# Kernel tuning notes

Measured on AMD Instinct MI355X. Metric: run time of the kernel, lower is better.

Reference implementation:

```python
import jax, jax.numpy as jnp
import numpy as np

B, S, D = 4, 2048, 512
H, DK, DV = 8, 64, 64
ALPHA = 0.6
MAX_ITERS = 3
EPS = 1e-9


def setup_inputs() -> dict:
    key = jax.random.key(0)
    ks = jax.random.split(key, 9)
    scale = 1.0 / np.sqrt(D)
    return {
        "x": jax.random.normal(ks[0], (B, S, D), dtype=jnp.float32),
        "Wq": jax.random.normal(ks[1], (D, H * DK), dtype=jnp.float32) * scale,
        "bq": jnp.zeros((H * DK,), dtype=jnp.float32),
        "Wk": jax.random.normal(ks[2], (D, H * DK), dtype=jnp.float32) * scale,
        "bk": jnp.zeros((H * DK,), dtype=jnp.float32),
        "Wv": jax.random.normal(ks[3], (D, H * DV), dtype=jnp.float32) * scale,
        "bv": jnp.zeros((H * DV,), dtype=jnp.float32),
        "Wo": jax.random.normal(ks[4], (H * DV, D), dtype=jnp.float32) * scale,
        "bo": jnp.zeros((D,), dtype=jnp.float32),
    }


def reference(x, Wq, bq, Wk, bk, Wv, bv, Wo, bo):
    # QKV projections -> [B, H, S, dk]
    q = (x @ Wq + bq).reshape(B, S, H, DK).transpose(0, 2, 1, 3)
    k = (x @ Wk + bk).reshape(B, S, H, DK).transpose(0, 2, 1, 3)
    v = (x @ Wv + bv).reshape(B, S, H, DV).transpose(0, 2, 1, 3)

    # scaled dot-product scores: [B, H, S, S]
    scores = jnp.einsum("bhqd,bhkd->bhqk", q, k) / jnp.sqrt(jnp.float32(DK))
    w = jax.nn.softmax(scores, axis=-1)

    # iterative sparsification: threshold_t = 1 / (alpha^t * N), then renormalize
    n = jnp.float32(S)
    for t in range(MAX_ITERS):
        thr = 1.0 / ((ALPHA ** t) * n)
        w = jnp.where(w >= thr, w, 0.0)
        w = w / (jnp.sum(w, axis=-1, keepdims=True) + EPS)

    # attend and project out
    out = jnp.einsum("bhqk,bhkd->bhqd", w, v)          # [B, H, S, dv]
    out = out.transpose(0, 2, 1, 3).reshape(B, S, H * DV)
    return out @ Wo + bo
```

## Files before the change

### kernel.cpp

```cpp
#include <hip/hip_runtime.h>
#include <hip/hip_bf16.h>
#include <math.h>

#define NB 4
#define NS 2048
#define ND 512
#define NH 8
#define NDK 64
#define NDV 64

typedef __attribute__((ext_vector_type(8))) short short8;
typedef __attribute__((ext_vector_type(4))) float f32x4;
typedef __attribute__((ext_vector_type(4))) unsigned int u32x4;

__device__ __forceinline__ unsigned short f2bfu(float f) {
  unsigned int u = __builtin_bit_cast(unsigned int, f);
  unsigned int rounding = 0x7fffu + ((u >> 16) & 1u);
  return (unsigned short)((u + rounding) >> 16);
}
__device__ __forceinline__ float bfu2f(unsigned short u) {
  return __builtin_bit_cast(float, (unsigned int)u << 16);
}


__global__ void k_make_xcat(const float* __restrict__ in, unsigned short* __restrict__ out,
                            int n4) {
  int i = blockIdx.x * 256 + threadIdx.x;
  if (i >= n4) return;
  int row = i >> 7, col = (i & 127) * 4;
  float4 f = reinterpret_cast<const float4*>(in)[i];
  ushort4 h, l;
  h.x = f2bfu(f.x); h.y = f2bfu(f.y); h.z = f2bfu(f.z); h.w = f2bfu(f.w);
  l.x = f2bfu(f.x - bfu2f(h.x)); l.y = f2bfu(f.y - bfu2f(h.y));
  l.z = f2bfu(f.z - bfu2f(h.z)); l.w = f2bfu(f.w - bfu2f(h.w));
  ushort4* o = reinterpret_cast<ushort4*>(out + (size_t)row * 1536);
  o[col / 4] = h;
  o[(col + 512) / 4] = h;
  o[(col + 1024) / 4] = l;
}

__global__ void k_transpose_split(const float* __restrict__ src, unsigned short* __restrict__ dst,
                                  int R, int C) {
  __shared__ float t[32][33];
  int bx = blockIdx.x * 32, by = blockIdx.y * 32;
  int tx = threadIdx.x, ty = threadIdx.y;
  for (int i = 0; i < 32; i += 8)
    t[ty + i][tx] = src[(size_t)(by + ty + i) * C + bx + tx];
  __syncthreads();
  for (int i = 0; i < 32; i += 8) {
    float f = t[tx][ty + i];
    unsigned short h = f2bfu(f);
    unsigned short l = f2bfu(f - bfu2f(h));
    size_t base = (size_t)(bx + ty + i) * (3 * R) + by + tx;
    dst[base] = h;
    dst[base + R] = l;
    dst[base + 2 * R] = h;
  }
}

template <int MODE>
__global__ __launch_bounds__(256) void k_gemm_nt(
    const unsigned short* __restrict__ A, const unsigned short* __restrict__ Bt,
    const float* __restrict__ bias, void* __restrict__ outp, unsigned short* __restrict__ outlo,
    int M, int N, int K) {
  __shared__ __align__(16) unsigned short As[64][88];
  __shared__ __align__(16) unsigned short Bs[64][88];
  const int tid = threadIdx.x;
  const int m0 = blockIdx.y * 64;
  const int n0 = blockIdx.x * 64;
  const int wave = tid >> 6, lane = tid & 63;
  const int lm = lane & 15, lg = lane >> 4;

  f32x4 acc[4];
  for (int n = 0; n < 4; n++) acc[n] = (f32x4){0.f, 0.f, 0.f, 0.f};

  for (int k0 = 0; k0 < K; k0 += 64) {
    for (int it = 0; it < 2; it++) {
      int c = tid + it * 256;
      int row = c >> 3, col = (c & 7) * 8;
      *reinterpret_cast<short8*>(&As[row][col]) =
          *reinterpret_cast<const short8*>(A + (size_t)(m0 + row) * K + k0 + col);
      *reinterpret_cast<short8*>(&Bs[row][col]) =
          *reinterpret_cast<const short8*>(Bt + (size_t)(n0 + row) * K + k0 + col);
    }
    __syncthreads();
#pragma unroll
    for (int ks = 0; ks < 2; ks++) {
      short8 a = *reinterpret_cast<const short8*>(&As[wave * 16 + lm][ks * 32 + lg * 8]);
#pragma unroll
      for (int n = 0; n < 4; n++) {
        short8 b = *reinterpret_cast<const short8*>(&Bs[n * 16 + lm][ks * 32 + lg * 8]);
        acc[n] = __builtin_amdgcn_mfma_f32_16x16x32_bf16(a, b, acc[n], 0, 0, 0);
      }
    }
    __syncthreads();
  }

#pragma unroll
  for (int n = 0; n < 4; n++) {
    int gn = n0 + n * 16 + lm;
    float bv = bias[gn];
#pragma unroll
    for (int r = 0; r < 4; r++) {
      int gm = m0 + wave * 16 + lg * 4 + r;
      float v = acc[n][r] + bv;
      if (MODE == 3) {
        reinterpret_cast<float*>(outp)[(size_t)gm * ND + gn] = v;
      } else {
        int b = gm >> 11, s = gm & (NS - 1);
        int h = gn >> 6, d = gn & 63;
        unsigned short hb = f2bfu(v);
        unsigned short lb = f2bfu(v - bfu2f(hb));
        size_t idx;
        if (MODE == 0)
          idx = (((size_t)b * NH + h) * NS + s) * NDK + d;
        else
          idx = (((size_t)b * NH + h) * NDV + d) * NS + s;
        reinterpret_cast<unsigned short*>(outp)[idx] = hb;
        outlo[idx] = lb;
      }
    }
  }
}

__global__ __launch_bounds__(512, 4) void k_sparse_attn(
    const unsigned short* __restrict__ Qh, const unsigned short* __restrict__ Ql,
    const unsigned short* __restrict__ Kh, const unsigned short* __restrict__ Kl,
    const unsigned short* __restrict__ Vth, const unsigned short* __restrict__ Vtl,
    unsigned short* __restrict__ attn) {
  __shared__ float part[5][8][16];
  __shared__ __align__(16) float red[8][16][68];

  const int tid = threadIdx.x;
  const int wave = tid >> 6, lane = tid & 63;
  const int lm = lane & 15, lg = lane >> 4;

  const int orig = blockIdx.x;
  const int blk = (orig & 7) * 512 + (orig >> 3);
  const int qt = blk & (NS / 16 - 1);
  const int bh = blk >> 7;
  const int q0 = qt * 16;

  const size_t qoff = ((size_t)bh * NS + q0) * NDK;
  const unsigned short* Kph = Kh + (size_t)bh * NS * NDK;
  const unsigned short* Kpl = Kl + (size_t)bh * NS * NDK;
  const unsigned short* Vph = Vth + (size_t)bh * NDV * NS;
  const unsigned short* Vpl = Vtl + (size_t)bh * NDV * NS;
  const int kvbase = wave * 256;

  f32x4 st[16];
  {
    short8 qh0 = *reinterpret_cast<const short8*>(Qh + qoff + lm * NDK + lg * 8);
    short8 qh1 = *reinterpret_cast<const short8*>(Qh + qoff + lm * NDK + 32 + lg * 8);
    short8 ql0 = *reinterpret_cast<const short8*>(Ql + qoff + lm * NDK + lg * 8);
    short8 ql1 = *reinterpret_cast<const short8*>(Ql + qoff + lm * NDK + 32 + lg * 8);
#pragma unroll
    for (int kt = 0; kt < 16; kt++) {
      size_t ko = (size_t)(kvbase + kt * 16) * NDK;
      const unsigned short* kh = Kph + ko + lm * NDK + lg * 8;
      const unsigned short* kl = Kpl + ko + lm * NDK + lg * 8;
      short8 ah0 = *reinterpret_cast<const short8*>(kh);
      short8 ah1 = *reinterpret_cast<const short8*>(kh + 32);
      short8 al0 = *reinterpret_cast<const short8*>(kl);
      short8 al1 = *reinterpret_cast<const short8*>(kl + 32);
      f32x4 a0 = (f32x4){0.f, 0.f, 0.f, 0.f};
      f32x4 a1 = (f32x4){0.f, 0.f, 0.f, 0.f};
      a0 = __builtin_amdgcn_mfma_f32_16x16x32_bf16(ah0, qh0, a0, 0, 0, 0);
      a1 = __builtin_amdgcn_mfma_f32_16x16x32_bf16(ah1, qh1, a1, 0, 0, 0);
      a0 = __builtin_amdgcn_mfma_f32_16x16x32_bf16(al0, qh0, a0, 0, 0, 0);
      a1 = __builtin_amdgcn_mfma_f32_16x16x32_bf16(al1, qh1, a1, 0, 0, 0);
      a0 = __builtin_amdgcn_mfma_f32_16x16x32_bf16(ah0, ql0, a0, 0, 0, 0);
      a1 = __builtin_amdgcn_mfma_f32_16x16x32_bf16(ah1, ql1, a1, 0, 0, 0);
      st[kt] = (a0 + a1) * 0.125f;
    }
  }

  float cut, inv;
  {
    float m = -1e30f;
#pragma unroll
    for (int kt = 0; kt < 16; kt++)
      m = fmaxf(m, fmaxf(fmaxf(st[kt][0], st[kt][1]), fmaxf(st[kt][2], st[kt][3])));
    m = fmaxf(m, __shfl_xor(m, 16));
    m = fmaxf(m, __shfl_xor(m, 32));
    if (lg == 0) part[0][wave][lm] = m;
    __syncthreads();
    float gm = -1e30f;
#pragma unroll
    for (int w = 0; w < 8; w++) gm = fmaxf(gm, part[0][w][lm]);

    float E = 0.f;
#pragma unroll
    for (int kt = 0; kt < 16; kt++) {
#pragma unroll
      for (int j = 0; j < 4; j++) {
        float e = __expf(st[kt][j] - gm);
        st[kt][j] = e;
        E += e;
      }
    }
    E += __shfl_xor(E, 16);
    E += __shfl_xor(E, 32);
    if (lg == 0) part[1][wave][lm] = E;
    __syncthreads();
    float gE = 0.f;
#pragma unroll
    for (int w = 0; w < 8; w++) gE += part[1][w][lm];

    const float thr[3] = {1.0f / 2048.0f, 1.0f / (0.6f * 2048.0f), 1.0f / (0.36f * 2048.0f)};
    float Dd = 1.0f;
    cut = 0.f;
#pragma unroll
    for (int t = 0; t < 3; t++) {
      cut = fmaxf(cut, thr[t] * Dd * gE);
      float S = 0.f;
#pragma unroll
      for (int kt = 0; kt < 16; kt++) {
#pragma unroll
        for (int j = 0; j < 4; j++) S += (st[kt][j] >= cut) ? st[kt][j] : 0.f;
      }
      S += __shfl_xor(S, 16);
      S += __shfl_xor(S, 32);
      if (lg == 0) part[2 + t][wave][lm] = S;
      __syncthreads();
      float gS = 0.f;
#pragma unroll
      for (int w = 0; w < 8; w++) gS += part[2 + t][w][lm];
      Dd = gS / gE + 1e-9f * Dd;
    }
    inv = 1.0f / (gE * Dd);
  }

  unsigned int Hp[16][2], Lp[16][2];
#pragma unroll
  for (int kt = 0; kt < 16; kt++) {
#pragma unroll
    for (int rp = 0; rp < 2; rp++) {
      float w0 = st[kt][2 * rp], w1 = st[kt][2 * rp + 1];
      w0 = (w0 >= cut) ? w0 * inv : 0.f;
      w1 = (w1 >= cut) ? w1 * inv : 0.f;
      unsigned int h0 = f2bfu(w0), h1 = f2bfu(w1);
      Hp[kt][rp] = h0 | (h1 << 16);
      unsigned int l0 = f2bfu(w0 - bfu2f((unsigned short)h0));
      unsigned int l1 = f2bfu(w1 - bfu2f((unsigned short)h1));
      Lp[kt][rp] = l0 | (l1 << 16);
    }
  }

  {
    const int e_lane = lm + 32 * (lg & 1);
    const int o_lane = e_lane + 16;
    const bool selB = (lane & 32) != 0;
    f32x4 acc[4];
#pragma unroll
    for (int dt = 0; dt < 4; dt++) acc[dt] = (f32x4){0.f, 0.f, 0.f, 0.f};
#pragma unroll
    for (int wi = 0; wi < 8; wi++) {
      unsigned int a0 = (unsigned)__shfl((int)Hp[2 * wi][0], e_lane);
      unsigned int a1 = (unsigned)__shfl((int)Hp[2 * wi][1], e_lane);
      unsigned int a2 = (unsigned)__shfl((int)Hp[2 * wi][0], o_lane);
      unsigned int a3 = (unsigned)__shfl((int)Hp[2 * wi][1], o_lane);
      unsigned int b0 = (unsigned)__shfl((int)Hp[2 * wi + 1][0], e_lane);
      unsigned int b1 = (unsigned)__shfl((int)Hp[2 * wi + 1][1], e_lane);
      unsigned int b2 = (unsigned)__shfl((int)Hp[2 * wi + 1][0], o_lane);
      unsigned int b3 = (unsigned)__shfl((int)Hp[2 * wi + 1][1], o_lane);
      u32x4 hw = (u32x4){selB ? b0 : a0, selB ? b1 : a1, selB ? b2 : a2, selB ? b3 : a3};
      a0 = (unsigned)__shfl((int)Lp[2 * wi][0], e_lane);
      a1 = (unsigned)__shfl((int)Lp[2 * wi][1], e_lane);
      a2 = (unsigned)__shfl((int)Lp[2 * wi][0], o_lane);
      a3 = (unsigned)__shfl((int)Lp[2 * wi][1], o_lane);
      b0 = (unsigned)__shfl((int)Lp[2 * wi + 1][0], e_lane);
      b1 = (unsigned)__shfl((int)Lp[2 * wi + 1][1], e_lane);
      b2 = (unsigned)__shfl((int)Lp[2 * wi + 1][0], o_lane);
      b3 = (unsigned)__shfl((int)Lp[2 * wi + 1][1], o_lane);
      u32x4 lw = (u32x4){selB ? b0 : a0, selB ? b1 : a1, selB ? b2 : a2, selB ? b3 : a3};
      short8 Ah = __builtin_bit_cast(short8, hw);
      short8 Al = __builtin_bit_cast(short8, lw);
      const int co = kvbase + wi * 32 + lg * 8;
#pragma unroll
      for (int dt = 0; dt < 4; dt++) {
        short8 V0 = *reinterpret_cast<const short8*>(Vph + (size_t)(dt * 16 + lm) * NS + co);
        short8 V1 = *reinterpret_cast<const short8*>(Vpl + (size_t)(dt * 16 + lm) * NS + co);
        acc[dt] = __builtin_amdgcn_mfma_f32_16x16x32_bf16(Ah, V0, acc[dt], 0, 0, 0);
        acc[dt] = __builtin_amdgcn_mfma_f32_16x16x32_bf16(Ah, V1, acc[dt], 0, 0, 0);
        acc[dt] = __builtin_amdgcn_mfma_f32_16x16x32_bf16(Al, V0, acc[dt], 0, 0, 0);
      }
    }
#pragma unroll
    for (int dt = 0; dt < 4; dt++)
#pragma unroll
      for (int rr = 0; rr < 4; rr++) red[wave][lg * 4 + rr][dt * 16 + lm] = acc[dt][rr];
  }
  __syncthreads();

  {
    const int q = tid >> 5;
    const int dv0 = (tid & 31) * 2;
    const int b = bh >> 3, h = bh & 7;
    const int s = q0 + q;
    size_t base = ((size_t)b * NS + s) * 1536;
#pragma unroll
    for (int k2 = 0; k2 < 2; k2++) {
      int dv = dv0 + k2;
      float v = 0.f;
#pragma unroll
      for (int w = 0; w < 8; w++) v += red[w][q][dv];
      int c = h * 64 + dv;
      unsigned short hb = f2bfu(v);
      unsigned short lb = f2bfu(v - bfu2f(hb));
      attn[base + c] = hb;
      attn[base + c + 512] = hb;
      attn[base + c + 1024] = lb;
    }
  }
}


extern "C" void kernel_launch(void* const* d_in, const int* in_sizes, int n_in,
                              void* d_out, int out_size, void* d_ws, size_t ws_size,
                              hipStream_t stream) {
  const float* x  = (const float*)d_in[0];
  const float* Wq = (const float*)d_in[1];
  const float* bq = (const float*)d_in[2];
  const float* Wk = (const float*)d_in[3];
  const float* bk = (const float*)d_in[4];
  const float* Wv = (const float*)d_in[5];
  const float* bv = (const float*)d_in[6];
  const float* Wo = (const float*)d_in[7];
  const float* bo = (const float*)d_in[8];

  char* ws = (char*)d_ws;
  size_t off = 0;
  auto alloc = [&](size_t bytes) {
    char* p = ws + off;
    off += (bytes + 255) & ~(size_t)255;
    return p;
  };
  const int M = NB * NS;
  unsigned short* xcat = (unsigned short*)alloc((size_t)M * 1536 * 2);
  unsigned short* wqC  = (unsigned short*)alloc((size_t)512 * 1536 * 2);
  unsigned short* wkC  = (unsigned short*)alloc((size_t)512 * 1536 * 2);
  unsigned short* wvC  = (unsigned short*)alloc((size_t)512 * 1536 * 2);
  unsigned short* woC  = (unsigned short*)alloc((size_t)512 * 1536 * 2);
  unsigned short* Qhi  = (unsigned short*)alloc((size_t)M * 512 * 2);
  unsigned short* Qlo  = (unsigned short*)alloc((size_t)M * 512 * 2);
  unsigned short* Khi  = (unsigned short*)alloc((size_t)M * 512 * 2);
  unsigned short* Klo  = (unsigned short*)alloc((size_t)M * 512 * 2);
  unsigned short* Vthi = (unsigned short*)alloc((size_t)M * 512 * 2);
  unsigned short* Vtlo = (unsigned short*)alloc((size_t)M * 512 * 2);
  unsigned short* attn = xcat;

  k_make_xcat<<<(M * 512 / 4 + 255) / 256, 256, 0, stream>>>(x, xcat, M * 512 / 4);

  dim3 tg(16, 16), tb(32, 8);
  k_transpose_split<<<tg, tb, 0, stream>>>(Wq, wqC, ND, NH * NDK);
  k_transpose_split<<<tg, tb, 0, stream>>>(Wk, wkC, ND, NH * NDK);
  k_transpose_split<<<tg, tb, 0, stream>>>(Wv, wvC, ND, NH * NDV);
  k_transpose_split<<<tg, tb, 0, stream>>>(Wo, woC, NH * NDV, ND);

  dim3 gg(512 / 64, M / 64);
  k_gemm_nt<0><<<gg, 256, 0, stream>>>(xcat, wqC, bq, Qhi, Qlo, M, 512, 1536);
  k_gemm_nt<0><<<gg, 256, 0, stream>>>(xcat, wkC, bk, Khi, Klo, M, 512, 1536);
  k_gemm_nt<2><<<gg, 256, 0, stream>>>(xcat, wvC, bv, Vthi, Vtlo, M, 512, 1536);

  k_sparse_attn<<<NB * NH * (NS / 16), 512, 0, stream>>>(Qhi, Qlo, Khi, Klo, Vthi, Vtlo, attn);

  k_gemm_nt<3><<<gg, 256, 0, stream>>>(attn, woC, bo, d_out, nullptr, M, 512, 1536);
}
```

Measured before the change: 805.5 us.

## Split attention key range across 16 waves and compute packed weights inline

Doubles the attention block to 1024 threads (16 waves), so each wave handles 128 keys and keeps half as many score registers. The bf16 hi/lo weight packing now happens inside the PV loop instead of in a separate stored array, which further cuts register pressure. The final cross-wave reduction reads float2 and writes packed 32-bit words. The aim is more resident waves and better latency hiding, at the cost of more partial-sum traffic through shared memory and more barrier participants.

```diff
diff --git a/kernel.cpp b/kernel.cpp
--- a/kernel.cpp
+++ b/kernel.cpp
@@ -123,13 +123,13 @@
   }
 }
 
-__global__ __launch_bounds__(512, 4) void k_sparse_attn(
+__global__ __launch_bounds__(1024, 8) void k_sparse_attn(
     const unsigned short* __restrict__ Qh, const unsigned short* __restrict__ Ql,
     const unsigned short* __restrict__ Kh, const unsigned short* __restrict__ Kl,
     const unsigned short* __restrict__ Vth, const unsigned short* __restrict__ Vtl,
     unsigned short* __restrict__ attn) {
-  __shared__ float part[5][8][16];
-  __shared__ __align__(16) float red[8][16][68];
+  __shared__ float part[5][16][16];
+  __shared__ __align__(16) float red[16][16][68];
 
   const int tid = threadIdx.x;
   const int wave = tid >> 6, lane = tid & 63;
@@ -146,16 +146,16 @@
   const unsigned short* Kpl = Kl + (size_t)bh * NS * NDK;
   const unsigned short* Vph = Vth + (size_t)bh * NDV * NS;
   const unsigned short* Vpl = Vtl + (size_t)bh * NDV * NS;
-  const int kvbase = wave * 256;
-
-  f32x4 st[16];
+  const int kvbase = wave * 128;
+
+  f32x4 st[8];
   {
     short8 qh0 = *reinterpret_cast<const short8*>(Qh + qoff + lm * NDK + lg * 8);
     short8 qh1 = *reinterpret_cast<const short8*>(Qh + qoff + lm * NDK + 32 + lg * 8);
     short8 ql0 = *reinterpret_cast<const short8*>(Ql + qoff + lm * NDK + lg * 8);
     short8 ql1 = *reinterpret_cast<const short8*>(Ql + qoff + lm * NDK + 32 + lg * 8);
 #pragma unroll
-    for (int kt = 0; kt < 16; kt++) {
+    for (int kt = 0; kt < 8; kt++) {
       size_t ko = (size_t)(kvbase + kt * 16) * NDK;
       const unsigned short* kh = Kph + ko + lm * NDK + lg * 8;
       const unsigned short* kl = Kpl + ko + lm * NDK + lg * 8;
@@ -179,7 +179,7 @@
   {
     float m = -1e30f;
 #pragma unroll
-    for (int kt = 0; kt < 16; kt++)
+    for (int kt = 0; kt < 8; kt++)
       m = fmaxf(m, fmaxf(fmaxf(st[kt][0], st[kt][1]), fmaxf(st[kt][2], st[kt][3])));
     m = fmaxf(m, __shfl_xor(m, 16));
     m = fmaxf(m, __shfl_xor(m, 32));
@@ -187,11 +187,11 @@
     __syncthreads();
     float gm = -1e30f;
 #pragma unroll
-    for (int w = 0; w < 8; w++) gm = fmaxf(gm, part[0][w][lm]);
+    for (int w = 0; w < 16; w++) gm = fmaxf(gm, part[0][w][lm]);
 
     float E = 0.f;
 #pragma unroll
-    for (int kt = 0; kt < 16; kt++) {
+    for (int kt = 0; kt < 8; kt++) {
 #pragma unroll
       for (int j = 0; j < 4; j++) {
         float e = __expf(st[kt][j] - gm);
@@ -205,7 +205,7 @@
     __syncthreads();
     float gE = 0.f;
 #pragma unroll
-    for (int w = 0; w < 8; w++) gE += part[1][w][lm];
+    for (int w = 0; w < 16; w++) gE += part[1][w][lm];
 
     const float thr[3] = {1.0f / 2048.0f, 1.0f / (0.6f * 2048.0f), 1.0f / (0.36f * 2048.0f)};
     float Dd = 1.0f;
@@ -215,7 +215,7 @@
       cut = fmaxf(cut, thr[t] * Dd * gE);
       float S = 0.f;
 #pragma unroll
-      for (int kt = 0; kt < 16; kt++) {
+      for (int kt = 0; kt < 8; kt++) {
 #pragma unroll
         for (int j = 0; j < 4; j++) S += (st[kt][j] >= cut) ? st[kt][j] : 0.f;
       }
@@ -225,26 +225,10 @@
       __syncthreads();
       float gS = 0.f;
 #pragma unroll
-      for (int w = 0; w < 8; w++) gS += part[2 + t][w][lm];
+      for (int w = 0; w < 16; w++) gS += part[2 + t][w][lm];
       Dd = gS / gE + 1e-9f * Dd;
     }
     inv = 1.0f / (gE * Dd);
-  }
-
-  unsigned int Hp[16][2], Lp[16][2];
-#pragma unroll
-  for (int kt = 0; kt < 16; kt++) {
-#pragma unroll
-    for (int rp = 0; rp < 2; rp++) {
-      float w0 = st[kt][2 * rp], w1 = st[kt][2 * rp + 1];
-      w0 = (w0 >= cut) ? w0 * inv : 0.f;
-      w1 = (w1 >= cut) ? w1 * inv : 0.f;
-      unsigned int h0 = f2bfu(w0), h1 = f2bfu(w1);
-      Hp[kt][rp] = h0 | (h1 << 16);
-      unsigned int l0 = f2bfu(w0 - bfu2f((unsigned short)h0));
-      unsigned int l1 = f2bfu(w1 - bfu2f((unsigned short)h1));
-      Lp[kt][rp] = l0 | (l1 << 16);
-    }
   }
 
   {
@@ -255,24 +239,40 @@
 #pragma unroll
     for (int dt = 0; dt < 4; dt++) acc[dt] = (f32x4){0.f, 0.f, 0.f, 0.f};
 #pragma unroll
-    for (int wi = 0; wi < 8; wi++) {
-      unsigned int a0 = (unsigned)__shfl((int)Hp[2 * wi][0], e_lane);
-      unsigned int a1 = (unsigned)__shfl((int)Hp[2 * wi][1], e_lane);
-      unsigned int a2 = (unsigned)__shfl((int)Hp[2 * wi][0], o_lane);
-      unsigned int a3 = (unsigned)__shfl((int)Hp[2 * wi][1], o_lane);
-      unsigned int b0 = (unsigned)__shfl((int)Hp[2 * wi + 1][0], e_lane);
-      unsigned int b1 = (unsigned)__shfl((int)Hp[2 * wi + 1][1], e_lane);
-      unsigned int b2 = (unsigned)__shfl((int)Hp[2 * wi + 1][0], o_lane);
-      unsigned int b3 = (unsigned)__shfl((int)Hp[2 * wi + 1][1], o_lane);
+    for (int wi = 0; wi < 4; wi++) {
+      unsigned int cw[8];
+#pragma unroll
+      for (int half = 0; half < 2; half++) {
+        f32x4 s = st[2 * wi + half];
+#pragma unroll
+        for (int rp = 0; rp < 2; rp++) {
+          float w0 = s[2 * rp], w1 = s[2 * rp + 1];
+          w0 = (w0 >= cut) ? w0 * inv : 0.f;
+          w1 = (w1 >= cut) ? w1 * inv : 0.f;
+          unsigned int h0 = f2bfu(w0), h1 = f2bfu(w1);
+          cw[half * 2 + rp] = h0 | (h1 << 16);
+          unsigned int l0 = f2bfu(w0 - bfu2f((unsigned short)h0));
+          unsigned int l1 = f2bfu(w1 - bfu2f((unsigned short)h1));
+          cw[4 + half * 2 + rp] = l0 | (l1 << 16);
+        }
+      }
+      unsigned int a0 = (unsigned)__shfl((int)cw[0], e_lane);
+      unsigned int a1 = (unsigned)__shfl((int)cw[1], e_lane);
+      unsigned int a2 = (unsigned)__shfl((int)cw[0], o_lane);
+      unsigned int a3 = (unsigned)__shfl((int)cw[1], o_lane);
+      unsigned int b0 = (unsigned)__shfl((int)cw[2], e_lane);
+      unsigned int b1 = (unsigned)__shfl((int)cw[3], e_lane);
+      unsigned int b2 = (unsigned)__shfl((int)cw[2], o_lane);
+      unsigned int b3 = (unsigned)__shfl((int)cw[3], o_lane);
       u32x4 hw = (u32x4){selB ? b0 : a0, selB ? b1 : a1, selB ? b2 : a2, selB ? b3 : a3};
-      a0 = (unsigned)__shfl((int)Lp[2 * wi][0], e_lane);
-      a1 = (unsigned)__shfl((int)Lp[2 * wi][1], e_lane);
-      a2 = (unsigned)__shfl((int)Lp[2 * wi][0], o_lane);
-      a3 = (unsigned)__shfl((int)Lp[2 * wi][1], o_lane);
-      b0 = (unsigned)__shfl((int)Lp[2 * wi + 1][0], e_lane);
-      b1 = (unsigned)__shfl((int)Lp[2 * wi + 1][1], e_lane);
-      b2 = (unsigned)__shfl((int)Lp[2 * wi + 1][0], o_lane);
-      b3 = (unsigned)__shfl((int)Lp[2 * wi + 1][1], o_lane);
+      a0 = (unsigned)__shfl((int)cw[4], e_lane);
+      a1 = (unsigned)__shfl((int)cw[5], e_lane);
+      a2 = (unsigned)__shfl((int)cw[4], o_lane);
+      a3 = (unsigned)__shfl((int)cw[5], o_lane);
+      b0 = (unsigned)__shfl((int)cw[6], e_lane);
+      b1 = (unsigned)__shfl((int)cw[7], e_lane);
+      b2 = (unsigned)__shfl((int)cw[6], o_lane);
+      b3 = (unsigned)__shfl((int)cw[7], o_lane);
       u32x4 lw = (u32x4){selB ? b0 : a0, selB ? b1 : a1, selB ? b2 : a2, selB ? b3 : a3};
       short8 Ah = __builtin_bit_cast(short8, hw);
       short8 Al = __builtin_bit_cast(short8, lw);
@@ -293,25 +293,27 @@
   }
   __syncthreads();
 
-  {
+  if (tid < 512) {
     const int q = tid >> 5;
     const int dv0 = (tid & 31) * 2;
     const int b = bh >> 3, h = bh & 7;
     const int s = q0 + q;
-    size_t base = ((size_t)b * NS + s) * 1536;
-#pragma unroll
-    for (int k2 = 0; k2 < 2; k2++) {
-      int dv = dv0 + k2;
-      float v = 0.f;
-#pragma unroll
-      for (int w = 0; w < 8; w++) v += red[w][q][dv];
-      int c = h * 64 + dv;
-      unsigned short hb = f2bfu(v);
-      unsigned short lb = f2bfu(v - bfu2f(hb));
-      attn[base + c] = hb;
-      attn[base + c + 512] = hb;
-      attn[base + c + 1024] = lb;
-    }
+    float v0 = 0.f, v1 = 0.f;
+#pragma unroll
+    for (int w = 0; w < 16; w++) {
+      float2 rr = *reinterpret_cast<const float2*>(&red[w][q][dv0]);
+      v0 += rr.x;
+      v1 += rr.y;
+    }
+    unsigned short h0 = f2bfu(v0), h1 = f2bfu(v1);
+    unsigned int hw = (unsigned int)h0 | ((unsigned int)h1 << 16);
+    unsigned int lw = (unsigned int)f2bfu(v0 - bfu2f(h0)) |
+                      ((unsigned int)f2bfu(v1 - bfu2f(h1)) << 16);
+    unsigned int* out32 = reinterpret_cast<unsigned int*>(attn + ((size_t)b * NS + s) * 1536);
+    int cwi = h * 32 + (dv0 >> 1);
+    out32[cwi] = hw;
+    out32[cwi + 256] = hw;
+    out32[cwi + 512] = lw;
   }
 }
 
@@ -363,7 +365,7 @@
   k_gemm_nt<0><<<gg, 256, 0, stream>>>(xcat, wkC, bk, Khi, Klo, M, 512, 1536);
   k_gemm_nt<2><<<gg, 256, 0, stream>>>(xcat, wvC, bv, Vthi, Vtlo, M, 512, 1536);
 
-  k_sparse_attn<<<NB * NH * (NS / 16), 512, 0, stream>>>(Qhi, Qlo, Khi, Klo, Vthi, Vtlo, attn);
+  k_sparse_attn<<<NB * NH * (NS / 16), 1024, 0, stream>>>(Qhi, Qlo, Khi, Klo, Vthi, Vtlo, attn);
 
   k_gemm_nt<3><<<gg, 256, 0, stream>>>(attn, woC, bo, d_out, nullptr, M, 512, 1536);
 }
```

New measurement: 897.3 us. +11.4%, slower.
